# Optimization experiments

Hardware: AMD Instinct MI355X
Metric: run time of the kernel (lower is better)

## Reference

```python
import jax, jax.numpy as jnp
import numpy as np

N = 50000      # nodes
F = 128        # feature_dim
H = 128        # hidden_dim
E = 1_600_000  # edges
G = 64         # graphs in batch
A = 8          # n_actions


def setup_inputs() -> dict:
    key = jax.random.key(0)
    ks = jax.random.split(key, 12)
    s = 0.05
    return {
        "x": jax.random.normal(ks[0], (N, F), jnp.float32),
        "edge_attr": jax.random.uniform(ks[1], (E, 1), jnp.float32),
        "W_e1": jax.random.normal(ks[2], (3, 1), jnp.float32) * s,
        "b_e1": jnp.zeros((1,), jnp.float32),
        "W_e2": jax.random.normal(ks[3], (1, 1), jnp.float32) * s,
        "b_e2": jnp.zeros((1,), jnp.float32),
        "W_gcn": jax.random.normal(ks[4], (F, H), jnp.float32) * s,
        "b_gcn": jnp.zeros((H,), jnp.float32),
        "W2": jax.random.normal(ks[5], (H, H), jnp.float32) * s,
        "b2": jnp.zeros((H,), jnp.float32),
        "W3": jax.random.normal(ks[6], (H, A), jnp.float32) * s,
        "b3": jnp.zeros((A,), jnp.float32),
        "edge_index": jax.random.randint(ks[7], (2, E), 0, N, jnp.int64),
        "batch": jnp.sort(jax.random.randint(ks[8], (N,), 0, G, jnp.int64)),
    }


def reference(x, edge_attr, W_e1, b_e1, W_e2, b_e2, W_gcn, b_gcn, W2, b2, W3, b3, edge_index, batch):
    # edge MLP: input is [src, dst, edge_attr] per edge -> (E, 3)
    e_feat = jnp.concatenate([edge_index.T.astype(x.dtype), edge_attr], axis=1)
    h = jax.nn.relu(e_feat @ W_e1 + b_e1)
    w = jax.nn.sigmoid(h @ W_e2 + b_e2)[:, 0]  # (E,)

    # GCNConv: add self-loops (weight 1), symmetric normalization
    loop = jnp.arange(N)
    row = jnp.concatenate([edge_index[0], loop])      # source
    col = jnp.concatenate([edge_index[1], loop])      # target
    w_all = jnp.concatenate([w, jnp.ones((N,), w.dtype)])
    deg = jax.ops.segment_sum(w_all, col, num_segments=N)
    safe_deg = jnp.where(deg > 0, deg, 1.0)
    dis = jnp.where(deg > 0, 1.0 / jnp.sqrt(safe_deg), 0.0)  # deg^-1/2, inf->0
    norm = dis[row] * w_all * dis[col]                # (E+N,)

    xw = x @ W_gcn                                    # (N, H)
    msg = norm[:, None] * xw[row]                     # (E+N, H) gather
    conv = jax.ops.segment_sum(msg, col, num_segments=N) + b_gcn  # scatter
    h1 = jax.nn.relu(conv)

    # global_mean_pool over batch index
    sums = jax.ops.segment_sum(h1, batch, num_segments=G)
    cnt = jax.ops.segment_sum(jnp.ones((N,), h1.dtype), batch, num_segments=G)
    pooled = sums / jnp.maximum(cnt, 1.0)[:, None]    # (G, H)

    h2 = jax.nn.relu(pooled @ W2 + b2)
    return h2 @ W3 + b3                               # (G, A)
```

## Files before the change

### kernel.cpp

```cpp
#include <hip/hip_runtime.h>
#include <hip/hip_fp16.h>
#include <math.h>

#define GB 64
#define AD 8
#define NC2 256
#define BSH 6
#define BS  64
#define NBMAX 1024

typedef _Float16 half8 __attribute__((ext_vector_type(8)));
typedef float    f32x4 __attribute__((ext_vector_type(4)));

__global__ __launch_bounds__(512) void k_hist2(const int* __restrict__ ei,
                                               int* __restrict__ H2,
                                               int E, int ce, int NB) {
    __shared__ int h[NBMAX];
    int c = blockIdx.x;
    for (int b = threadIdx.x; b < NB; b += 512) h[b] = 0;
    __syncthreads();
    int e0 = c * ce, e1 = min(e0 + ce, E);
    int nv = (e1 - e0) & ~3;
    const int4* dst4 = (const int4*)(ei + E + e0);
    for (int v = threadIdx.x; v < (nv >> 2); v += 512) {
        int4 d = dst4[v];
        atomicAdd(&h[d.x >> BSH], 1);
        atomicAdd(&h[d.y >> BSH], 1);
        atomicAdd(&h[d.z >> BSH], 1);
        atomicAdd(&h[d.w >> BSH], 1);
    }
    for (int e = e0 + nv + threadIdx.x; e < e1; e += 512)
        atomicAdd(&h[ei[E + e] >> BSH], 1);
    __syncthreads();
    for (int b = threadIdx.x; b < NB; b += 512)
        H2[(size_t)c * NB + b] = h[b];
}

__global__ __launch_bounds__(256) void k_cscan(int* __restrict__ H2,
                                               int* __restrict__ cntB,
                                               int NB, int nc) {
    __shared__ int ssum[256];
    int b = blockIdx.x;
    int t = threadIdx.x;
    int v = (t < nc) ? H2[(size_t)t * NB + b] : 0;
    ssum[t] = v;
    __syncthreads();
    for (int s = 1; s < 256; s <<= 1) {
        int tmp = (t >= s) ? ssum[t - s] : 0;
        __syncthreads();
        ssum[t] += tmp;
        __syncthreads();
    }
    if (t < nc) H2[(size_t)t * NB + b] = ssum[t] - v;
    if (t == 255) cntB[b] = ssum[255];
}

__global__ __launch_bounds__(1024) void k_bscan(const int* __restrict__ cntB,
                                                int* __restrict__ bb,
                                                int* __restrict__ rowptr,
                                                float* __restrict__ psum,
                                                int NB, int n, int E) {
    __shared__ int sm[1024];
    int t = threadIdx.x;
    for (int z = t; z < GB * 128; z += 1024) psum[z] = 0.0f;
    int v = (t < NB) ? cntB[t] : 0;
    sm[t] = v;
    __syncthreads();
    for (int s = 1; s < 1024; s <<= 1) {
        int tmp = (t >= s) ? sm[t - s] : 0;
        __syncthreads();
        sm[t] += tmp;
        __syncthreads();
    }
    if (t < NB) bb[t] = sm[t] - v;
    if (t == NB - 1) bb[NB] = sm[t];
    if (t == 0) rowptr[n] = E;
}

__global__ __launch_bounds__(512) void k_fill2(const int* __restrict__ ei,
                                               const float* __restrict__ attr,
                                               const float* __restrict__ W_e1,
                                               const float* __restrict__ b_e1,
                                               const float* __restrict__ W_e2,
                                               const float* __restrict__ b_e2,
                                               const int* __restrict__ bb,
                                               const int* __restrict__ H2,
                                               int2* __restrict__ rec,
                                               int E, int ce, int NB) {
    __shared__ int off[NBMAX];
    int c = blockIdx.x;
    for (int b = threadIdx.x; b < NB; b += 512)
        off[b] = bb[b] + H2[(size_t)c * NB + b];
    __syncthreads();
    float w1s = W_e1[0], w1d = W_e1[1], w1a = W_e1[2], bb1 = b_e1[0];
    float w2 = W_e2[0], bb2 = b_e2[0];
    int e0 = c * ce, e1 = min(e0 + ce, E);
    int nv = (e1 - e0) & ~3;
    const int4*   src4 = (const int4*)(ei + e0);
    const int4*   dst4 = (const int4*)(ei + E + e0);
    const float4* att4 = (const float4*)(attr + e0);
    for (int v = threadIdx.x; v < (nv >> 2); v += 512) {
        int4 sv = src4[v];
        int4 dv = dst4[v];
        float4 av = att4[v];
        int   ss[4] = {sv.x, sv.y, sv.z, sv.w};
        int   dd[4] = {dv.x, dv.y, dv.z, dv.w};
        float aa[4] = {av.x, av.y, av.z, av.w};
        #pragma unroll
        for (int k = 0; k < 4; k++) {
            float h = fmaxf((float)ss[k] * w1s + (float)dd[k] * w1d + aa[k] * w1a + bb1, 0.0f);
            float w = 1.0f / (1.0f + expf(-(h * w2 + bb2)));
            int pos = atomicAdd(&off[dd[k] >> BSH], 1);
            int2 rv;
            rv.x = ss[k] | ((dd[k] & (BS - 1)) << 16);
            rv.y = __float_as_int(w);
            rec[pos] = rv;
        }
    }
    for (int e = e0 + nv + threadIdx.x; e < e1; e += 512) {
        int d = ei[E + e];
        int s = ei[e];
        float h = fmaxf((float)s * w1s + (float)d * w1d + attr[e] * w1a + bb1, 0.0f);
        float w = 1.0f / (1.0f + expf(-(h * w2 + bb2)));
        int pos = atomicAdd(&off[d >> BSH], 1);
        int2 rv;
        rv.x = s | ((d & (BS - 1)) << 16);
        rv.y = __float_as_int(w);
        rec[pos] = rv;
    }
}

__global__ __launch_bounds__(256) void k_bucket(const int2* __restrict__ rec,
                                                const int* __restrict__ bb,
                                                unsigned int* __restrict__ rec3,
                                                int* __restrict__ rowptr,
                                                float* __restrict__ dis, int n) {
    __shared__ int   cntL[BS];
    __shared__ float degL[BS];
    __shared__ int   pfx[BS];
    __shared__ int   cnt2[BS];
    int b = blockIdx.x;
    int t = threadIdx.x;
    if (t < BS) { cntL[t] = 0; degL[t] = 1.0f; cnt2[t] = 0; }
    __syncthreads();
    int s0 = bb[b], s1 = bb[b + 1];
    for (int j = s0 + t; j < s1; j += 256) {
        int2 rv = rec[j];
        int dl = (rv.x >> 16) & (BS - 1);
        atomicAdd(&cntL[dl], 1);
        atomicAdd(&degL[dl], __int_as_float(rv.y));
    }
    __syncthreads();
    if (t == 0) {
        int acc = 0;
        for (int k = 0; k < BS; k++) { pfx[k] = acc; acc += cntL[k]; }
    }
    __syncthreads();
    int lo = b << BSH;
    if (t < BS) {
        int i = lo + t;
        if (i < n) {
            rowptr[i] = s0 + pfx[t];
            dis[i] = rsqrtf(degL[t]);
        }
    }
    for (int j = s0 + t; j < s1; j += 256) {
        int2 rv = rec[j];
        int dl = (rv.x >> 16) & (BS - 1);
        int r = atomicAdd(&cnt2[dl], 1);
        unsigned int hh = (unsigned int)__half_as_ushort(
                              __float2half(__int_as_float(rv.y)));
        rec3[s0 + pfx[dl] + r] = (unsigned int)(rv.x & 0xFFFF) | (hh << 16);
    }
}

__global__ __launch_bounds__(256) void k_xw(const float* __restrict__ x,
                                            const float* __restrict__ Wg,
                                            const float* __restrict__ dis,
                                            __half* __restrict__ xwh, int n) {
    __shared__ _Float16 Wh[128 * 136];
    int tid = threadIdx.x;
    for (int idx = tid; idx < 128 * 128; idx += 256) {
        int k = idx >> 7, c = idx & 127;
        Wh[c * 136 + k] = (_Float16)Wg[idx];
    }
    __syncthreads();

    int lane = tid & 63;
    int w = tid >> 6;
    int n16 = lane & 15;
    int quad = lane >> 4;

    #pragma unroll
    for (int hf = 0; hf < 2; hf++) {
        int r0 = blockIdx.x * 128 + hf * 64 + w * 16;
        if (r0 >= n) break;
        int arow = min(r0 + n16, n - 1);
        const float* xrow = x + (size_t)arow * 128;

        f32x4 acc[8];
        #pragma unroll
        for (int nt = 0; nt < 8; nt++) acc[nt] = (f32x4){0.f, 0.f, 0.f, 0.f};

        #pragma unroll
        for (int kk = 0; kk < 4; kk++) {
            int k0 = kk * 32 + quad * 8;
            float4 f0 = *(const float4*)(xrow + k0);
            float4 f1 = *(const float4*)(xrow + k0 + 4);
            half8 a;
            a[0] = (_Float16)f0.x; a[1] = (_Float16)f0.y;
            a[2] = (_Float16)f0.z; a[3] = (_Float16)f0.w;
            a[4] = (_Float16)f1.x; a[5] = (_Float16)f1.y;
            a[6] = (_Float16)f1.z; a[7] = (_Float16)f1.w;
            #pragma unroll
            for (int nt = 0; nt < 8; nt++) {
                half8 b = *(const half8*)&Wh[(nt * 16 + n16) * 136 + k0];
                acc[nt] = __builtin_amdgcn_mfma_f32_16x16x32_f16(a, b, acc[nt], 0, 0, 0);
            }
        }

        #pragma unroll
        for (int r = 0; r < 4; r++) {
            int row = r0 + quad * 4 + r;
            if (row < n) {
                float dv = dis[row];
                #pragma unroll
                for (int nt = 0; nt < 8; nt++)
                    xwh[(size_t)row * 128 + nt * 16 + n16] = __float2half(acc[nt][r] * dv);
            }
        }
    }
}

__global__ __launch_bounds__(256) void k_gather(const unsigned int* __restrict__ rec3,
                                                const int* __restrict__ rowptr,
                                                const float* __restrict__ dis,
                                                const __half* __restrict__ xh,
                                                const float* __restrict__ bg,
                                                const int* __restrict__ batch,
                                                float* __restrict__ psum, int n) {
    __shared__ float ps4[4][128];
    __shared__ int   gix[4];
    int wave = threadIdx.x >> 6;
    int lane = threadIdx.x & 63;
    int g = lane >> 4;
    int q = lane & 15;
    int i = blockIdx.x * 4 + wave;
    bool valid = (i < n);

    int st = 0, m = 0;
    float di = 0.0f;
    float acc[8];
    #pragma unroll
    for (int k = 0; k < 8; k++) acc[k] = 0.0f;

    if (valid) {
        st = rowptr[i];
        m = rowptr[i + 1] - st;
        di = dis[i];
        uint4 sr = *(const uint4*)(xh + (size_t)i * 128 + q * 8);
        const __half2* hp = (const __half2*)&sr;
        float sc = (g == 0) ? 1.0f : 0.0f;
        #pragma unroll
        for (int k = 0; k < 4; k++) {
            float2 f = __half22float2(hp[k]);
            acc[2 * k]     = sc * f.x;
            acc[2 * k + 1] = sc * f.y;
        }
        for (int base = 0; base < m; base += 64) {
            int kk = min(64, m - base);
            unsigned int rv = 0u;
            if (lane < kk) rv = rec3[st + base + lane];
            int jn = (kk + 3) >> 2;
            for (int j = 0; j < jn; j += 8) {
                float cf[8];
                uint4 rw[8];
                #pragma unroll
                for (int u = 0; u < 8; u++) {
                    int idx = ((j + u) << 2) + g;
                    unsigned int rvj = (unsigned int)__builtin_amdgcn_ds_bpermute(
                                           idx << 2, (int)rv);
                    int s = rvj & 0xFFFF;
                    cf[u] = __half2float(__ushort_as_half((unsigned short)(rvj >> 16)));
                    rw[u] = *(const uint4*)(xh + (size_t)s * 128 + q * 8);
                }
                #pragma unroll
                for (int u = 0; u < 8; u++) {
                    const __half2* rp = (const __half2*)&rw[u];
                    #pragma unroll
                    for (int k = 0; k < 4; k++) {
                        float2 f = __half22float2(rp[k]);
                        acc[2 * k]     += cf[u] * f.x;
                        acc[2 * k + 1] += cf[u] * f.y;
                    }
                }
            }
        }
        #pragma unroll
        for (int k = 0; k < 8; k++) {
            acc[k] += __shfl_xor(acc[k], 16);
            acc[k] += __shfl_xor(acc[k], 32);
        }
    }

    if (lane == 0) gix[wave] = valid ? batch[i] : -1;
    if (valid && g == 0) {
        float4 b0 = *(const float4*)(bg + q * 8);
        float4 b1 = *(const float4*)(bg + q * 8 + 4);
        const float* bp = (const float*)&b0;
        #pragma unroll
        for (int k = 0; k < 4; k++)
            ps4[wave][q * 8 + k] = fmaxf(di * acc[k] + bp[k], 0.0f);
        bp = (const float*)&b1;
        #pragma unroll
        for (int k = 0; k < 4; k++)
            ps4[wave][q * 8 + 4 + k] = fmaxf(di * acc[4 + k] + bp[k], 0.0f);
    }
    __syncthreads();
    int t = threadIdx.x;
    if (t < 128) {
        int g0 = gix[0];
        if (g0 >= 0 && gix[1] == g0 && gix[2] == g0 && gix[3] == g0) {
            float s = ps4[0][t] + ps4[1][t] + ps4[2][t] + ps4[3][t];
            atomicAdd(&psum[g0 * 128 + t], s);
        } else {
            #pragma unroll
            for (int w2 = 0; w2 < 4; w2++)
                if (gix[w2] >= 0)
                    atomicAdd(&psum[gix[w2] * 128 + t], ps4[w2][t]);
        }
    }
}

__device__ __forceinline__ int lbound(const int* __restrict__ a, int n, int v) {
    int lo = 0, hi = n;
    while (lo < hi) {
        int mid = (lo + hi) >> 1;
        if (a[mid] < v) lo = mid + 1; else hi = mid;
    }
    return lo;
}

__global__ __launch_bounds__(128) void k_head(const float* __restrict__ psum,
                                              const int* __restrict__ batch,
                                              const float* __restrict__ W2,
                                              const float* __restrict__ b2,
                                              const float* __restrict__ W3,
                                              const float* __restrict__ b3,
                                              float* __restrict__ out, int n) {
    __shared__ float pl[128];
    __shared__ float h2s[128];
    __shared__ float cS;
    int g = blockIdx.x;
    int t = threadIdx.x;
    if (t == 0) {
        int s = lbound(batch, n, g);
        int e = lbound(batch, n, g + 1);
        cS = fmaxf((float)(e - s), 1.0f);
    }
    __syncthreads();
    pl[t] = psum[g * 128 + t] / cS;
    __syncthreads();
    float acc = b2[t];
    for (int k = 0; k < 128; k++) acc += pl[k] * W2[k * 128 + t];
    h2s[t] = fmaxf(acc, 0.0f);
    __syncthreads();
    if (t < AD) {
        float o = b3[t];
        for (int k = 0; k < 128; k++) o += h2s[k] * W3[k * AD + t];
        out[g * AD + t] = o;
    }
}

extern "C" void kernel_launch(void* const* d_in, const int* in_sizes, int n_in,
                              void* d_out, int out_size, void* d_ws, size_t ws_size,
                              hipStream_t stream) {
    const float* x        = (const float*)d_in[0];
    const float* edge_attr= (const float*)d_in[1];
    const float* W_e1     = (const float*)d_in[2];
    const float* b_e1     = (const float*)d_in[3];
    const float* W_e2     = (const float*)d_in[4];
    const float* b_e2     = (const float*)d_in[5];
    const float* W_gcn    = (const float*)d_in[6];
    const float* b_gcn    = (const float*)d_in[7];
    const float* W2       = (const float*)d_in[8];
    const float* b2       = (const float*)d_in[9];
    const float* W3       = (const float*)d_in[10];
    const float* b3       = (const float*)d_in[11];
    const int*   ei       = (const int*)d_in[12];
    const int*   batch    = (const int*)d_in[13];
    float* out = (float*)d_out;

    const int E  = in_sizes[12] / 2;
    const int n  = in_sizes[13];
    const int NB = (n + BS - 1) >> BSH;
    const int ce = (((E + NC2 - 1) / NC2) + 3) & ~3;

    char* p = (char*)d_ws;
    __half* xwh   = (__half*)p;  p += (size_t)n * 128 * sizeof(__half);
    int*    H2    = (int*)p;     p += (size_t)n * 128 * sizeof(__half);
    int2*   rec   = (int2*)p;    p += (size_t)E * sizeof(int2);
    unsigned int* rec3 = (unsigned int*)p; p += (size_t)E * sizeof(unsigned int);
    float*  dis   = (float*)p;   p += (size_t)n * sizeof(float);
    float*  psum  = (float*)p;   p += (size_t)GB * 128 * sizeof(float);
    float*  pcnt  = (float*)p;   p += (size_t)GB * sizeof(float);
    int*    rowptr= (int*)p;     p += (size_t)(n + 1) * sizeof(int);
    int*    cntB  = (int*)p;     p += (size_t)NBMAX * sizeof(int);
    int*    bb    = (int*)p;     p += (size_t)(NBMAX + 1) * sizeof(int);
    (void)pcnt;

    k_hist2<<<NC2, 512, 0, stream>>>(ei, H2, E, ce, NB);
    k_cscan<<<NB, 256, 0, stream>>>(H2, cntB, NB, NC2);
    k_bscan<<<1, 1024, 0, stream>>>(cntB, bb, rowptr, psum, NB, n, E);
    k_fill2<<<NC2, 512, 0, stream>>>(ei, edge_attr, W_e1, b_e1, W_e2, b_e2,
                                     bb, H2, rec, E, ce, NB);
    k_bucket<<<NB, 256, 0, stream>>>(rec, bb, rec3, rowptr, dis, n);
    k_xw<<<(n + 127) / 128, 256, 0, stream>>>(x, W_gcn, dis, xwh, n);
    k_gather<<<(n + 3) / 4, 256, 0, stream>>>(rec3, rowptr, dis, xwh,
                                              b_gcn, batch, psum, n);
    k_head<<<GB, 128, 0, stream>>>(psum, batch, W2, b2, W3, b3, out, n);
}
```

Before: 232.0 us.

## Process four nodes per wave in gather and accumulate pool sums in registers

The gather kernel now has each wave handle four consecutive nodes instead of one. It keeps the per-graph pooled sum in registers and flushes it with global atomics only when the graph index changes, which removes the shared-memory staging and block-wide barrier. It also batches the bpermute index reads before the row loads, adds a scheduling barrier, uses packed float2 FMAs, and sets launch bounds with an occupancy hint. The grid shrinks by four times, so there are fewer waves to hide gather latency. Per-wave work becomes serial across the four nodes.

```diff
diff --git a/kernel.cpp b/kernel.cpp
--- a/kernel.cpp
+++ b/kernel.cpp
@@ -11,6 +11,7 @@
 
 typedef _Float16 half8 __attribute__((ext_vector_type(8)));
 typedef float    f32x4 __attribute__((ext_vector_type(4)));
+typedef float    f32x2 __attribute__((ext_vector_type(2)));
 
 __global__ __launch_bounds__(512) void k_hist2(const int* __restrict__ ei,
                                                int* __restrict__ H2,
@@ -232,103 +233,114 @@
     }
 }
 
-__global__ __launch_bounds__(256) void k_gather(const unsigned int* __restrict__ rec3,
-                                                const int* __restrict__ rowptr,
-                                                const float* __restrict__ dis,
-                                                const __half* __restrict__ xh,
-                                                const float* __restrict__ bg,
-                                                const int* __restrict__ batch,
-                                                float* __restrict__ psum, int n) {
-    __shared__ float ps4[4][128];
-    __shared__ int   gix[4];
-    int wave = threadIdx.x >> 6;
+__global__ __launch_bounds__(256, 4) void k_gather(const unsigned int* __restrict__ rec3,
+                                                   const int* __restrict__ rowptr,
+                                                   const float* __restrict__ dis,
+                                                   const __half* __restrict__ xh,
+                                                   const float* __restrict__ bg,
+                                                   const int* __restrict__ batch,
+                                                   float* __restrict__ psum, int n) {
+    int wid = blockIdx.x * 4 + (threadIdx.x >> 6);
     int lane = threadIdx.x & 63;
     int g = lane >> 4;
     int q = lane & 15;
-    int i = blockIdx.x * 4 + wave;
-    bool valid = (i < n);
-
-    int st = 0, m = 0;
-    float di = 0.0f;
-    float acc[8];
+    int i0 = wid * 4;
+    if (i0 >= n) return;
+    int iend = min(i0 + 4, n);
+
+    float bq[8];
+    {
+        float4 b0 = *(const float4*)(bg + q * 8);
+        float4 b1 = *(const float4*)(bg + q * 8 + 4);
+        bq[0] = b0.x; bq[1] = b0.y; bq[2] = b0.z; bq[3] = b0.w;
+        bq[4] = b1.x; bq[5] = b1.y; bq[6] = b1.z; bq[7] = b1.w;
+    }
+    float pp[8];
     #pragma unroll
-    for (int k = 0; k < 8; k++) acc[k] = 0.0f;
-
-    if (valid) {
-        st = rowptr[i];
-        m = rowptr[i + 1] - st;
-        di = dis[i];
-        uint4 sr = *(const uint4*)(xh + (size_t)i * 128 + q * 8);
-        const __half2* hp = (const __half2*)&sr;
-        float sc = (g == 0) ? 1.0f : 0.0f;
-        #pragma unroll
-        for (int k = 0; k < 4; k++) {
-            float2 f = __half22float2(hp[k]);
-            acc[2 * k]     = sc * f.x;
-            acc[2 * k + 1] = sc * f.y;
-        }
+    for (int k = 0; k < 8; k++) pp[k] = 0.0f;
+    int cur_g = batch[i0];
+
+    for (int i = i0; i < iend; ++i) {
+        int st = rowptr[i];
+        int m  = rowptr[i + 1] - st;
+        float di = dis[i];
+
+        f32x2 acc2[4];
+        {
+            uint4 sr = *(const uint4*)(xh + (size_t)i * 128 + q * 8);
+            const __half2* hp = (const __half2*)&sr;
+            float sc = (g == 0) ? 1.0f : 0.0f;
+            #pragma unroll
+            for (int k = 0; k < 4; k++) {
+                float2 f = __half22float2(hp[k]);
+                acc2[k] = (f32x2){sc * f.x, sc * f.y};
+            }
+        }
+
         for (int base = 0; base < m; base += 64) {
             int kk = min(64, m - base);
             unsigned int rv = 0u;
             if (lane < kk) rv = rec3[st + base + lane];
             int jn = (kk + 3) >> 2;
             for (int j = 0; j < jn; j += 8) {
+                unsigned int rvj[8];
+                #pragma unroll
+                for (int u = 0; u < 8; u++) {
+                    int idx = ((j + u) << 2) + g;
+                    rvj[u] = (unsigned int)__builtin_amdgcn_ds_bpermute(idx << 2, (int)rv);
+                }
                 float cf[8];
                 uint4 rw[8];
                 #pragma unroll
                 for (int u = 0; u < 8; u++) {
-                    int idx = ((j + u) << 2) + g;
-                    unsigned int rvj = (unsigned int)__builtin_amdgcn_ds_bpermute(
-                                           idx << 2, (int)rv);
-                    int s = rvj & 0xFFFF;
-                    cf[u] = __half2float(__ushort_as_half((unsigned short)(rvj >> 16)));
+                    int s = rvj[u] & 0xFFFF;
+                    cf[u] = __half2float(__ushort_as_half((unsigned short)(rvj[u] >> 16)));
                     rw[u] = *(const uint4*)(xh + (size_t)s * 128 + q * 8);
                 }
+                __builtin_amdgcn_sched_barrier(0);
                 #pragma unroll
                 for (int u = 0; u < 8; u++) {
                     const __half2* rp = (const __half2*)&rw[u];
                     #pragma unroll
                     for (int k = 0; k < 4; k++) {
                         float2 f = __half22float2(rp[k]);
-                        acc[2 * k]     += cf[u] * f.x;
-                        acc[2 * k + 1] += cf[u] * f.y;
+                        acc2[k] += cf[u] * (f32x2){f.x, f.y};
                     }
                 }
             }
         }
+
+        float accs[8];
+        #pragma unroll
+        for (int k = 0; k < 4; k++) {
+            accs[2 * k]     = acc2[k][0];
+            accs[2 * k + 1] = acc2[k][1];
+        }
         #pragma unroll
         for (int k = 0; k < 8; k++) {
-            acc[k] += __shfl_xor(acc[k], 16);
-            acc[k] += __shfl_xor(acc[k], 32);
-        }
-    }
-
-    if (lane == 0) gix[wave] = valid ? batch[i] : -1;
-    if (valid && g == 0) {
-        float4 b0 = *(const float4*)(bg + q * 8);
-        float4 b1 = *(const float4*)(bg + q * 8 + 4);
-        const float* bp = (const float*)&b0;
-        #pragma unroll
-        for (int k = 0; k < 4; k++)
-            ps4[wave][q * 8 + k] = fmaxf(di * acc[k] + bp[k], 0.0f);
-        bp = (const float*)&b1;
-        #pragma unroll
-        for (int k = 0; k < 4; k++)
-            ps4[wave][q * 8 + 4 + k] = fmaxf(di * acc[4 + k] + bp[k], 0.0f);
-    }
-    __syncthreads();
-    int t = threadIdx.x;
-    if (t < 128) {
-        int g0 = gix[0];
-        if (g0 >= 0 && gix[1] == g0 && gix[2] == g0 && gix[3] == g0) {
-            float s = ps4[0][t] + ps4[1][t] + ps4[2][t] + ps4[3][t];
-            atomicAdd(&psum[g0 * 128 + t], s);
-        } else {
+            accs[k] += __shfl_xor(accs[k], 16);
+            accs[k] += __shfl_xor(accs[k], 32);
+        }
+
+        int gi = batch[i];
+        if (gi != cur_g) {
+            if (g == 0) {
+                #pragma unroll
+                for (int k = 0; k < 8; k++)
+                    atomicAdd(&psum[cur_g * 128 + q * 8 + k], pp[k]);
+            }
             #pragma unroll
-            for (int w2 = 0; w2 < 4; w2++)
-                if (gix[w2] >= 0)
-                    atomicAdd(&psum[gix[w2] * 128 + t], ps4[w2][t]);
-        }
+            for (int k = 0; k < 8; k++) pp[k] = 0.0f;
+            cur_g = gi;
+        }
+        #pragma unroll
+        for (int k = 0; k < 8; k++)
+            pp[k] += fmaxf(di * accs[k] + bq[k], 0.0f);
+    }
+    if (g == 0) {
+        #pragma unroll
+        for (int k = 0; k < 8; k++)
+            atomicAdd(&psum[cur_g * 128 + q * 8 + k], pp[k]);
     }
 }
 
@@ -403,11 +415,9 @@
     unsigned int* rec3 = (unsigned int*)p; p += (size_t)E * sizeof(unsigned int);
     float*  dis   = (float*)p;   p += (size_t)n * sizeof(float);
     float*  psum  = (float*)p;   p += (size_t)GB * 128 * sizeof(float);
-    float*  pcnt  = (float*)p;   p += (size_t)GB * sizeof(float);
     int*    rowptr= (int*)p;     p += (size_t)(n + 1) * sizeof(int);
     int*    cntB  = (int*)p;     p += (size_t)NBMAX * sizeof(int);
     int*    bb    = (int*)p;     p += (size_t)(NBMAX + 1) * sizeof(int);
-    (void)pcnt;
 
     k_hist2<<<NC2, 512, 0, stream>>>(ei, H2, E, ce, NB);
     k_cscan<<<NB, 256, 0, stream>>>(H2, cntB, NB, NC2);
@@ -416,7 +426,7 @@
                                      bb, H2, rec, E, ce, NB);
     k_bucket<<<NB, 256, 0, stream>>>(rec, bb, rec3, rowptr, dis, n);
     k_xw<<<(n + 127) / 128, 256, 0, stream>>>(x, W_gcn, dis, xwh, n);
-    k_gather<<<(n + 3) / 4, 256, 0, stream>>>(rec3, rowptr, dis, xwh,
-                                              b_gcn, batch, psum, n);
+    k_gather<<<(n + 15) / 16, 256, 0, stream>>>(rec3, rowptr, dis, xwh,
+                                                b_gcn, batch, psum, n);
     k_head<<<GB, 128, 0, stream>>>(psum, batch, W2, b2, W3, b3, out, n);
 }
```

New measurement: 339.3 us. 46.2% more time.
